# Optimization experiments

Measured on AMD Instinct MI355X. Metric: run time of the kernel, lower is better.

The kernel has to match this reference:

```python
import jax, jax.numpy as jnp
import numpy as np

EPS = 1e-5

def layernorm(x, g, b):
    mu = jnp.mean(x, axis=-1, keepdims=True)
    var = jnp.var(x, axis=-1, keepdims=True)
    return (x - mu) * jax.lax.rsqrt(var + EPS) * g + b

DIM = 1024; CTX = 1024; HEADS = 12; DHEAD = 64; INNER = HEADS * DHEAD
B = 4; F = 2048; J = 1024

def setup_inputs() -> dict:
    key = jax.random.key(0)
    ks = jax.random.split(key, 8)
    s = lambda d: 1.0 / np.sqrt(d)
    return {
        "x": jax.random.normal(ks[0], (B, F, DIM), jnp.float32),
        "tab_x": jax.random.normal(ks[1], (B, J, CTX), jnp.float32),
        "tab_g": jnp.ones((CTX,), jnp.float32), "tab_b": jnp.zeros((CTX,), jnp.float32),
        "vid_g": jnp.ones((DIM,), jnp.float32), "vid_b": jnp.zeros((DIM,), jnp.float32),
        "Wq": jax.random.normal(ks[2], (DIM, INNER), jnp.float32) * s(DIM),
        "Wk": jax.random.normal(ks[3], (CTX, INNER), jnp.float32) * s(CTX),
        "Wv": jax.random.normal(ks[4], (CTX, INNER), jnp.float32) * s(CTX),
        "q_g": jnp.ones((INNER,), jnp.float32), "q_b": jnp.zeros((INNER,), jnp.float32),
        "k_g": jnp.ones((INNER,), jnp.float32), "k_b": jnp.zeros((INNER,), jnp.float32),
        "Wo": jax.random.normal(ks[5], (INNER, DIM), jnp.float32) * s(INNER),
        "bo": jnp.zeros((DIM,), jnp.float32),
    }

def reference(x, tab_x, tab_g, tab_b, vid_g, vid_b, Wq, Wk, Wv, q_g, q_b, k_g, k_b, Wo, bo):
    scale = DHEAD ** -0.5
    kv_in = layernorm(tab_x, tab_g, tab_b)                      # [b,j,ctx]
    q = layernorm(layernorm(x, vid_g, vid_b) @ Wq, q_g, q_b)    # [b,f,inner]
    k = layernorm(kv_in @ Wk, k_g, k_b)                         # [b,j,inner]
    v = kv_in @ Wv                                              # [b,j,inner]
    split = lambda t: t.reshape(t.shape[0], t.shape[1], HEADS, DHEAD).transpose(0, 2, 1, 3)
    q, k, v = split(q) * scale, split(k), split(v)              # [b,h,*,d]
    sim = jnp.einsum('bhid,bhjd->bhij', q, k)
    attn = jax.nn.softmax(sim, axis=-1)
    out = jnp.einsum('bhij,bhjd->bhid', attn, v)                # [b,h,f,d]
    out = out.transpose(0, 2, 1, 3).reshape(x.shape[0], x.shape[1], INNER)
    return out @ Wo + bo
```

## Files before the change

### kernel.cpp

```cpp
#include <hip/hip_runtime.h>

typedef unsigned short u16;
typedef float  f32x4   __attribute__((ext_vector_type(4)));
typedef float  f32x16  __attribute__((ext_vector_type(16)));
typedef __bf16 bf16x8  __attribute__((ext_vector_type(8)));
typedef u16    u16x4   __attribute__((ext_vector_type(4)));

#define DEV __device__ __forceinline__

DEV u16 f2bf(float f) {
  union { float f; unsigned u; } x; x.f = f;
  unsigned r = x.u + 0x7fffu + ((x.u >> 16) & 1u);
  return (u16)(r >> 16);
}
DEV float bf2f(u16 b) { union { unsigned u; float f; } c; c.u = (unsigned)b << 16; return c.f; }

DEV unsigned cvtpk(float lo, float hi) {
  unsigned r;
  asm("v_cvt_pk_bf16_f32 %0, %1, %2" : "=v"(r) : "v"(lo), "v"(hi));
  return r;
}

DEV f32x4 mfma16(bf16x8 a, bf16x8 b, f32x4 c) {
  return __builtin_amdgcn_mfma_f32_16x16x32_bf16(a, b, c, 0, 0, 0);
}
DEV f32x16 mfma32(bf16x8 a, bf16x8 b, f32x16 c) {
  return __builtin_amdgcn_mfma_f32_32x32x16_bf16(a, b, c, 0, 0, 0);
}

DEV void gload16(const void* g, void* l) {
  __builtin_amdgcn_global_load_lds(
      (__attribute__((address_space(1))) void*)g,
      (__attribute__((address_space(3))) void*)l, 16, 0, 0);
}

template<typename LOADER>
DEV void ln_body(LOADER load, const float* __restrict__ g, const float* __restrict__ bta,
                 u16* __restrict__ yrow, int C, float outscale, float* red)
{
  const int tid = threadIdx.x;
  const int n4 = C >> 2;
  f32x4 v = {0.f, 0.f, 0.f, 0.f};
  if (tid < n4) v = load(tid);
  float s1 = v[0] + v[1] + v[2] + v[3];
  float s2 = v[0]*v[0] + v[1]*v[1] + v[2]*v[2] + v[3]*v[3];
#pragma unroll
  for (int o = 32; o > 0; o >>= 1) {
    s1 += __shfl_xor(s1, o, 64);
    s2 += __shfl_xor(s2, o, 64);
  }
  const int lane = tid & 63, wv = tid >> 6;
  if (lane == 0) { red[wv] = s1; red[4 + wv] = s2; }
  __syncthreads();
  s1 = red[0] + red[1] + red[2] + red[3];
  s2 = red[4] + red[5] + red[6] + red[7];
  const float mu = s1 / C;
  const float rs = rsqrtf(s2 / C - mu * mu + 1e-5f);
  if (tid < n4) {
    f32x4 gg = *(const f32x4*)(g + 4 * tid);
    f32x4 bb = *(const f32x4*)(bta + 4 * tid);
    u16x4 o4;
#pragma unroll
    for (int j = 0; j < 4; ++j)
      o4[j] = f2bf(((v[j] - mu) * rs * gg[j] + bb[j]) * outscale);
    *(u16x4*)(yrow + 4 * tid) = o4;
  }
}

__global__ __launch_bounds__(256)
void prep(const float* __restrict__ Wq, const float* __restrict__ Wk,
          const float* __restrict__ Wv, const float* __restrict__ Wo,
          u16* __restrict__ WqT, u16* __restrict__ WkvT, u16* __restrict__ WoT,
          const float* __restrict__ tabx, const float* __restrict__ tab_g,
          const float* __restrict__ tab_b,
          const float* __restrict__ x, const float* __restrict__ vid_g,
          const float* __restrict__ vid_b,
          u16* __restrict__ kvn, u16* __restrict__ xn)
{
  __shared__ float t[32][33];
  __shared__ float red[8];
  const int bid = blockIdx.x;
  const int tid = threadIdx.x;
  if (bid < 3840) {
    const float* src; u16* dst; int K, N, k0, n0;
    if (bid < 3072) {
      const int w = bid / 768, r = bid % 768;
      src = (w == 0) ? Wq : (w == 1) ? Wk : Wv;
      dst = (w == 0) ? WqT : (w == 1) ? WkvT : WkvT + (size_t)768 * 1024;
      K = 1024; N = 768; k0 = (r % 32) * 32; n0 = (r / 32) * 32;
    } else {
      const int r = bid - 3072;
      src = Wo; dst = WoT;
      K = 768; N = 1024; k0 = (r % 24) * 32; n0 = (r / 24) * 32;
    }
    const int tx = tid & 31, ty = tid >> 5;
#pragma unroll
    for (int i = ty; i < 32; i += 8)
      t[i][tx] = src[(size_t)(k0 + i) * N + n0 + tx];
    __syncthreads();
#pragma unroll
    for (int i = ty; i < 32; i += 8)
      dst[(size_t)(n0 + i) * K + k0 + tx] = f2bf(t[tx][i]);
  } else {
    const int r = bid - 3840;
    const float* xr; const float *g, *bb; u16* y;
    if (r < 4096) { xr = tabx + (size_t)r * 1024; g = tab_g; bb = tab_b;
                    y = kvn + (size_t)r * 1024; }
    else { const int rr = r - 4096; xr = x + (size_t)rr * 1024; g = vid_g;
           bb = vid_b; y = xn + (size_t)rr * 1024; }
    ln_body([&](int i) { return *(const f32x4*)(xr + 4 * i); }, g, bb, y, 1024, 1.0f, red);
  }
}

__global__ __launch_bounds__(256)
void gemm_qkv(const u16* __restrict__ xn, const u16* __restrict__ kvn,
              const u16* __restrict__ WqT, const u16* __restrict__ WkvT,
              u16* __restrict__ q_pre, u16* __restrict__ k_pre, u16* __restrict__ vb)
{
  __shared__ __align__(16) u16 As[2][64 * 64];
  __shared__ __align__(16) u16 Bs[2][128 * 64];
  const int bid = blockIdx.x;
  const int tid  = threadIdx.x;
  const int lane = tid & 63;
  const int wave = tid >> 6;
  const bool isq = bid >= 768;
  const u16* A; const u16* Bt; int bm, bn;
  if (!isq) { A = kvn;  Bt = WkvT; bm = (bid & 63) * 64;  bn = (bid >> 6) * 128; }
  else { const int r = bid - 768; A = xn; Bt = WqT; bm = (r & 127) * 64; bn = (r >> 7) * 128; }
  const int wm = (wave >> 1) * 32;
  const int wn = (wave & 1) * 64;
  const int fr = lane & 15;
  const int fk = (lane >> 4) * 8;

  f32x4 acc[2][4] = {};
  const char* gA0 = (const char*)(A  + (size_t)bm * 1024);
  const char* gB0 = (const char*)(Bt + (size_t)bn * 1024);
  const size_t rowpitch = 2048;

  auto stage = [&](int buf, int k0) {
#pragma unroll
    for (int c = 0; c < 2; ++c) {
      const int off = tid * 16 + c * 4096;
      gload16(gA0 + (size_t)(off >> 7) * rowpitch + 2 * k0 + (off & 127),
              (char*)&As[buf][0] + wave * 1024 + c * 4096);
    }
#pragma unroll
    for (int c = 0; c < 4; ++c) {
      const int off = tid * 16 + c * 4096;
      gload16(gB0 + (size_t)(off >> 7) * rowpitch + 2 * k0 + (off & 127),
              (char*)&Bs[buf][0] + wave * 1024 + c * 4096);
    }
  };

  stage(0, 0);
  __syncthreads();
  int cur = 0;
  for (int t = 0; t < 16; ++t) {
    if (t + 1 < 16) stage(cur ^ 1, (t + 1) * 64);
    bf16x8 af[2][2], bg[4][2];
#pragma unroll
    for (int m = 0; m < 2; ++m)
#pragma unroll
      for (int kk = 0; kk < 2; ++kk)
        af[m][kk] = *(const bf16x8*)&As[cur][(wm + m * 16 + fr) * 64 + kk * 32 + fk];
#pragma unroll
    for (int n = 0; n < 4; ++n)
#pragma unroll
      for (int kk = 0; kk < 2; ++kk)
        bg[n][kk] = *(const bf16x8*)&Bs[cur][(wn + n * 16 + fr) * 64 + kk * 32 + fk];
#pragma unroll
    for (int kk = 0; kk < 2; ++kk)
#pragma unroll
      for (int m = 0; m < 2; ++m)
#pragma unroll
        for (int n = 0; n < 4; ++n)
          acc[m][n] = mfma16(af[m][kk], bg[n][kk], acc[m][n]);
    if (t + 1 < 16) __syncthreads();
    cur ^= 1;
  }

  const int orow0 = bm + wm + 4 * (lane >> 4);
  const int ocol0 = bn + wn + fr;
#pragma unroll
  for (int m = 0; m < 2; ++m)
#pragma unroll
    for (int n = 0; n < 4; ++n)
#pragma unroll
      for (int r = 0; r < 4; ++r) {
        const int row = orow0 + m * 16 + r;
        const int col = ocol0 + n * 16;
        const u16 v = f2bf(acc[m][n][r]);
        if (isq) q_pre[(size_t)row * 768 + col] = v;
        else if (bn < 768) k_pre[(size_t)row * 768 + col] = v;
        else               vb[(size_t)row * 768 + (col - 768)] = v;
      }
}

__global__ __launch_bounds__(256)
void ln_tv(const u16* __restrict__ k_pre, const float* __restrict__ k_g,
           const float* __restrict__ k_b, u16* __restrict__ kb,
           const u16* __restrict__ q_pre, const float* __restrict__ q_g,
           const float* __restrict__ q_b, u16* __restrict__ qb,
           const u16* __restrict__ vb, u16* __restrict__ vT)
{
  __shared__ u16 t[64][65];
  __shared__ float red[8];
  const int bid = blockIdx.x;
  const int tid = threadIdx.x;
  if (bid < 12288) {
    const bool isk = bid < 4096;
    const int row = isk ? bid : bid - 4096;
    const u16* xr = (isk ? k_pre : q_pre) + (size_t)row * 768;
    u16* y = (isk ? kb : qb) + (size_t)row * 768;
    const float sc = isk ? 1.0f : 0.125f * 1.44269504089f;
    ln_body([&](int i) {
      const u16x4 raw = *(const u16x4*)(xr + 4 * i);
      f32x4 v; 
#pragma unroll
      for (int j = 0; j < 4; ++j) v[j] = bf2f(raw[j]);
      return v;
    }, isk ? k_g : q_g, isk ? k_b : q_b, y, 768, sc, red);
  } else {
    const int r2 = bid - 12288;
    const int bh = r2 % 48, b = bh / 12, h = bh - b * 12;
    const int j0 = (r2 / 48) * 64;
    const int tx = tid & 63, ty = tid >> 6;
#pragma unroll
    for (int i = ty; i < 64; i += 4)
      t[i][tx] = vb[(size_t)(b * 1024 + j0 + i) * 768 + h * 64 + tx];
    __syncthreads();
#pragma unroll
    for (int i = ty; i < 64; i += 4)
      vT[((size_t)bh * 64 + i) * 1024 + j0 + tx] = t[tx][i];
  }
}

__global__ __launch_bounds__(256, 3)
void attn4(const u16* __restrict__ q, const u16* __restrict__ k,
           const u16* __restrict__ vT, u16* __restrict__ att)
{
  __shared__ __align__(16) u16 Ks[2][64 * 64];
  __shared__ __align__(16) u16 Vs[2][64 * 64];
  __shared__ __align__(16) u16 osm[4][32][72];

  const int bh = blockIdx.x;
  const int b = bh / 12, h = bh - b * 12;
  const int tid = threadIdx.x, lane = tid & 63, wave = tid >> 6;
  const int lq  = lane & 31;
  const int hi5 = lane >> 5;
  const int qrow = blockIdx.y * 128 + wave * 32 + lq;

  const u16* qp = q + (size_t)(b * 2048 + qrow) * 768 + h * 64 + hi5 * 8;
  bf16x8 qf[4];
#pragma unroll
  for (int ds = 0; ds < 4; ++ds) qf[ds] = *(const bf16x8*)(qp + ds * 16);

  f32x16 ot0 = {}, ot1 = {};
  float m = -1e30f, l = 0.f;

  const char* kg = (const char*)k + (size_t)(b * 1024) * 1536 + h * 128;
  const char* vg = (const char*)vT + (size_t)bh * 64 * 2048;
  const int rsw0 = (lq & 7) << 4;

  auto stage = [&](int buf, int j0) {
#pragma unroll
    for (int c = 0; c < 2; ++c) {
      const int o   = tid * 16 + c * 4096;
      const int row = o >> 7;
      const int scol = (o & 127) ^ ((row & 7) << 4);
      gload16(kg + (size_t)(j0 + row) * 1536 + scol,
              (char*)&Ks[buf][0] + wave * 1024 + c * 4096);
      gload16(vg + (size_t)row * 2048 + j0 * 2 + scol,
              (char*)&Vs[buf][0] + wave * 1024 + c * 4096);
    }
  };

  stage(0, 0);
  __syncthreads();
  int cur = 0;
  for (int t = 0; t < 16; ++t) {
    const int j0 = t * 64;
    if (t + 1 < 16) stage(cur ^ 1, j0 + 64);
    f32x16 st0 = {}, st1 = {};
    __builtin_amdgcn_s_setprio(1);
#pragma unroll
    for (int ds = 0; ds < 4; ++ds) {
      const int cb = ds * 32 + hi5 * 16;
      const bf16x8 k0 = *(const bf16x8*)((const char*)&Ks[cur][0] + lq * 128 + (cb ^ rsw0));
      const bf16x8 k1 = *(const bf16x8*)((const char*)&Ks[cur][0] + (lq + 32) * 128 + (cb ^ rsw0));
      st0 = mfma32(k0, qf[ds], st0);
      st1 = mfma32(k1, qf[ds], st1);
    }
    __builtin_amdgcn_s_setprio(0);
    float ta0 = fmaxf(st0[0], st1[0]), ta1 = fmaxf(st0[1], st1[1]);
    float ta2 = fmaxf(st0[2], st1[2]), ta3 = fmaxf(st0[3], st1[3]);
#pragma unroll
    for (int r = 4; r < 16; r += 4) {
      ta0 = fmaxf(fmaxf(st0[r],     st1[r]),     ta0);
      ta1 = fmaxf(fmaxf(st0[r + 1], st1[r + 1]), ta1);
      ta2 = fmaxf(fmaxf(st0[r + 2], st1[r + 2]), ta2);
      ta3 = fmaxf(fmaxf(st0[r + 3], st1[r + 3]), ta3);
    }
    float tmax = fmaxf(fmaxf(fmaxf(ta0, ta1), ta2), ta3);
    tmax = fmaxf(tmax, __shfl_xor(tmax, 32, 64));
    if (!__all(tmax - m <= 11.5416f)) {
      const float mn = fmaxf(m, tmax);
      const float sc = exp2f(m - mn);
      l *= sc;
#pragma unroll
      for (int r = 0; r < 16; ++r) { ot0[r] *= sc; ot1[r] *= sc; }
      m = mn;
    }
    float sa0 = 0.f, sa1 = 0.f, sa2 = 0.f, sa3 = 0.f;
#pragma unroll
    for (int r = 0; r < 16; r += 4) {
      float p0 = exp2f(st0[r]     - m); st0[r]     = p0; sa0 += p0;
      float p1 = exp2f(st0[r + 1] - m); st0[r + 1] = p1; sa1 += p1;
      float p2 = exp2f(st0[r + 2] - m); st0[r + 2] = p2; sa2 += p2;
      float p3 = exp2f(st0[r + 3] - m); st0[r + 3] = p3; sa3 += p3;
    }
#pragma unroll
    for (int r = 0; r < 16; r += 4) {
      float p0 = exp2f(st1[r]     - m); st1[r]     = p0; sa0 += p0;
      float p1 = exp2f(st1[r + 1] - m); st1[r + 1] = p1; sa1 += p1;
      float p2 = exp2f(st1[r + 2] - m); st1[r + 2] = p2; sa2 += p2;
      float p3 = exp2f(st1[r + 3] - m); st1[r + 3] = p3; sa3 += p3;
    }
    float ts = (sa0 + sa1) + (sa2 + sa3);
    ts += __shfl_xor(ts, 32, 64);
    l += ts;
    __builtin_amdgcn_s_setprio(1);
#pragma unroll
    for (int s4 = 0; s4 < 4; ++s4) {
      const int u = (s4 & 1) * 8;
      float a0, a1, a2, a3, b0, b1, b2, b3;
      if (s4 < 2) {
        a0 = st0[u]; a1 = st0[u + 1]; a2 = st0[u + 2]; a3 = st0[u + 3];
        b0 = st0[u + 4]; b1 = st0[u + 5]; b2 = st0[u + 6]; b3 = st0[u + 7];
      } else {
        a0 = st1[u]; a1 = st1[u + 1]; a2 = st1[u + 2]; a3 = st1[u + 3];
        b0 = st1[u + 4]; b1 = st1[u + 5]; b2 = st1[u + 6]; b3 = st1[u + 7];
      }
      const unsigned L0 = cvtpk(a0, a1), L1 = cvtpk(a2, a3);
      const unsigned H0 = cvtpk(b0, b1), H1 = cvtpk(b2, b3);
      const auto w02 = __builtin_amdgcn_permlane32_swap(L0, H0, false, false);
      const auto w13 = __builtin_amdgcn_permlane32_swap(L1, H1, false, false);
      union BU { unsigned w[4]; bf16x8 v; } pu;
      pu.w[0] = w02[0]; pu.w[1] = w13[0]; pu.w[2] = w02[1]; pu.w[3] = w13[1];
      const int cb = s4 * 32 + hi5 * 16;
      const bf16x8 v0 = *(const bf16x8*)((const char*)&Vs[cur][0] + lq * 128 + (cb ^ rsw0));
      const bf16x8 v1 = *(const bf16x8*)((const char*)&Vs[cur][0] + (lq + 32) * 128 + (cb ^ rsw0));
      ot0 = mfma32(v0, pu.v, ot0);
      ot1 = mfma32(v1, pu.v, ot1);
    }
    __builtin_amdgcn_s_setprio(0);
    if (t + 1 < 16) __syncthreads();
    cur ^= 1;
  }
  const float inv = 1.0f / l;
#pragma unroll
  for (int r = 0; r < 16; ++r) {
    const int d0 = (r & 3) + 8 * (r >> 2) + 4 * hi5;
    osm[wave][lq][d0]      = f2bf(ot0[r] * inv);
    osm[wave][lq][32 + d0] = f2bf(ot1[r] * inv);
  }
  __syncthreads();
  const int col = (lane & 7) * 8;
#pragma unroll
  for (int pass = 0; pass < 4; ++pass) {
    const int row = pass * 8 + (lane >> 3);
    const bf16x8 vv = *(const bf16x8*)&osm[wave][row][col];
    const int qg = blockIdx.y * 128 + wave * 32 + row;
    *(bf16x8*)(att + (size_t)(b * 2048 + qg) * 768 + h * 64 + col) = vv;
  }
}

__global__ __launch_bounds__(256)
void gemm_o(const u16* __restrict__ A, const u16* __restrict__ Bt,
            float* __restrict__ Cp, const float* __restrict__ bias)
{
  __shared__ __align__(16) u16 As[2][64 * 64];
  __shared__ __align__(16) u16 Bs[2][128 * 64];
  const int tid  = threadIdx.x;
  const int lane = tid & 63;
  const int wave = tid >> 6;
  const int bm = blockIdx.x * 64;
  const int bn = blockIdx.y * 128;
  const int wm = (wave >> 1) * 32;
  const int wn = (wave & 1) * 64;
  const int fr = lane & 15;
  const int fk = (lane >> 4) * 8;

  f32x4 acc[2][4] = {};
  const char* gA0 = (const char*)(A  + (size_t)bm * 768);
  const char* gB0 = (const char*)(Bt + (size_t)bn * 768);
  const size_t rowpitch = 1536;

  auto stage = [&](int buf, int k0) {
#pragma unroll
    for (int c = 0; c < 2; ++c) {
      const int off = tid * 16 + c * 4096;
      gload16(gA0 + (size_t)(off >> 7) * rowpitch + 2 * k0 + (off & 127),
              (char*)&As[buf][0] + wave * 1024 + c * 4096);
    }
#pragma unroll
    for (int c = 0; c < 4; ++c) {
      const int off = tid * 16 + c * 4096;
      gload16(gB0 + (size_t)(off >> 7) * rowpitch + 2 * k0 + (off & 127),
              (char*)&Bs[buf][0] + wave * 1024 + c * 4096);
    }
  };

  stage(0, 0);
  __syncthreads();
  int cur = 0;
  for (int t = 0; t < 12; ++t) {
    if (t + 1 < 12) stage(cur ^ 1, (t + 1) * 64);
    bf16x8 af[2][2], bg[4][2];
#pragma unroll
    for (int m = 0; m < 2; ++m)
#pragma unroll
      for (int kk = 0; kk < 2; ++kk)
        af[m][kk] = *(const bf16x8*)&As[cur][(wm + m * 16 + fr) * 64 + kk * 32 + fk];
#pragma unroll
    for (int n = 0; n < 4; ++n)
#pragma unroll
      for (int kk = 0; kk < 2; ++kk)
        bg[n][kk] = *(const bf16x8*)&Bs[cur][(wn + n * 16 + fr) * 64 + kk * 32 + fk];
#pragma unroll
    for (int kk = 0; kk < 2; ++kk)
#pragma unroll
      for (int m = 0; m < 2; ++m)
#pragma unroll
        for (int n = 0; n < 4; ++n)
          acc[m][n] = mfma16(af[m][kk], bg[n][kk], acc[m][n]);
    if (t + 1 < 12) __syncthreads();
    cur ^= 1;
  }

  const int orow0 = bm + wm + 4 * (lane >> 4);
  const int ocol0 = bn + wn + fr;
#pragma unroll
  for (int m = 0; m < 2; ++m)
#pragma unroll
    for (int n = 0; n < 4; ++n)
#pragma unroll
      for (int r = 0; r < 4; ++r) {
        const int row = orow0 + m * 16 + r;
        const int col = ocol0 + n * 16;
        Cp[(size_t)row * 1024 + col] = acc[m][n][r] + bias[col];
      }
}

extern "C" void kernel_launch(void* const* d_in, const int* in_sizes, int n_in,
                              void* d_out, int out_size, void* d_ws, size_t ws_size,
                              hipStream_t stream)
{
  const float* x     = (const float*)d_in[0];
  const float* tabx  = (const float*)d_in[1];
  const float* tab_g = (const float*)d_in[2];
  const float* tab_b = (const float*)d_in[3];
  const float* vid_g = (const float*)d_in[4];
  const float* vid_b = (const float*)d_in[5];
  const float* Wq    = (const float*)d_in[6];
  const float* Wk    = (const float*)d_in[7];
  const float* Wv    = (const float*)d_in[8];
  const float* q_g   = (const float*)d_in[9];
  const float* q_b   = (const float*)d_in[10];
  const float* k_g   = (const float*)d_in[11];
  const float* k_b   = (const float*)d_in[12];
  const float* Wo    = (const float*)d_in[13];
  const float* bo    = (const float*)d_in[14];

  char* ws = (char*)d_ws;
  const size_t O_WQT  = 0;
  const size_t O_WKVT = O_WQT  + (size_t)768 * 1024 * 2;
  const size_t O_WOT  = O_WKVT + (size_t)1536 * 1024 * 2;
  const size_t O_XN   = O_WOT  + (size_t)1024 * 768 * 2;
  const size_t O_KVN  = O_XN   + (size_t)8192 * 1024 * 2;
  const size_t O_QPRE = O_KVN  + (size_t)4096 * 1024 * 2;
  const size_t O_KPRE = O_QPRE + (size_t)8192 * 768 * 2;
  const size_t O_QB   = O_KPRE + (size_t)4096 * 768 * 2;
  const size_t O_KB   = O_QB   + (size_t)8192 * 768 * 2;
  const size_t O_VB   = O_KB   + (size_t)4096 * 768 * 2;
  const size_t O_VT   = O_VB   + (size_t)4096 * 768 * 2;
  const size_t O_ATT  = O_QPRE;

  u16*   WqT   = (u16*)(ws + O_WQT);
  u16*   WkvT  = (u16*)(ws + O_WKVT);
  u16*   WoT   = (u16*)(ws + O_WOT);
  u16*   xn    = (u16*)(ws + O_XN);
  u16*   kvn   = (u16*)(ws + O_KVN);
  u16*   q_pre = (u16*)(ws + O_QPRE);
  u16*   k_pre = (u16*)(ws + O_KPRE);
  u16*   qb    = (u16*)(ws + O_QB);
  u16*   kb    = (u16*)(ws + O_KB);
  u16*   vb    = (u16*)(ws + O_VB);
  u16*   vT    = (u16*)(ws + O_VT);
  u16*   attb  = (u16*)(ws + O_ATT);

  prep<<<16128, 256, 0, stream>>>(Wq, Wk, Wv, Wo, WqT, WkvT, WoT,
                                  tabx, tab_g, tab_b, x, vid_g, vid_b, kvn, xn);
  gemm_qkv<<<1536, 256, 0, stream>>>(xn, kvn, WqT, WkvT, q_pre, k_pre, vb);
  ln_tv<<<13056, 256, 0, stream>>>(k_pre, k_g, k_b, kb, q_pre, q_g, q_b, qb, vb, vT);
  attn4<<<dim3(48, 16), 256, 0, stream>>>(qb, kb, vT, attb);
  gemm_o<<<dim3(128, 8), 256, 0, stream>>>(attb, WoT, (float*)d_out, bo);
}
```

Baseline: 156.9 us.

## Swizzle GEMM LDS tiles, write V transposed from GEMM, relax pipeline barriers

The QKV and output GEMMs now XOR-swizzle their LDS tiles to avoid bank conflicts on fragment reads. The QKV GEMM writes V directly in the transposed per-head layout, which removes the separate transpose pass and the vb buffer. All three main loops switch from __syncthreads to explicit vmcnt waits plus raw s_barrier so prefetches stay in flight. The attention epilogue replaces a block barrier with an lgkmcnt wait. This risks subtle sync bugs if the vmcnt counts are wrong, and the transposed V stores are strided 8-byte writes.

```diff
diff --git a/kernel.cpp b/kernel.cpp
--- a/kernel.cpp
+++ b/kernel.cpp
@@ -115,7 +115,7 @@
 __global__ __launch_bounds__(256)
 void gemm_qkv(const u16* __restrict__ xn, const u16* __restrict__ kvn,
               const u16* __restrict__ WqT, const u16* __restrict__ WkvT,
-              u16* __restrict__ q_pre, u16* __restrict__ k_pre, u16* __restrict__ vb)
+              u16* __restrict__ q_pre, u16* __restrict__ k_pre, u16* __restrict__ vT)
 {
   __shared__ __align__(16) u16 As[2][64 * 64];
   __shared__ __align__(16) u16 Bs[2][128 * 64];
@@ -130,7 +130,7 @@
   const int wm = (wave >> 1) * 32;
   const int wn = (wave & 1) * 64;
   const int fr = lane & 15;
-  const int fk = (lane >> 4) * 8;
+  const int fkb = (lane >> 4) * 16;
 
   f32x4 acc[2][4] = {};
   const char* gA0 = (const char*)(A  + (size_t)bm * 1024);
@@ -141,33 +141,39 @@
 #pragma unroll
     for (int c = 0; c < 2; ++c) {
       const int off = tid * 16 + c * 4096;
-      gload16(gA0 + (size_t)(off >> 7) * rowpitch + 2 * k0 + (off & 127),
+      const int row = off >> 7;
+      const int scol = (off & 127) ^ ((row & 7) << 4);
+      gload16(gA0 + (size_t)row * rowpitch + 2 * k0 + scol,
               (char*)&As[buf][0] + wave * 1024 + c * 4096);
     }
 #pragma unroll
     for (int c = 0; c < 4; ++c) {
       const int off = tid * 16 + c * 4096;
-      gload16(gB0 + (size_t)(off >> 7) * rowpitch + 2 * k0 + (off & 127),
+      const int row = off >> 7;
+      const int scol = (off & 127) ^ ((row & 7) << 4);
+      gload16(gB0 + (size_t)row * rowpitch + 2 * k0 + scol,
               (char*)&Bs[buf][0] + wave * 1024 + c * 4096);
     }
   };
 
-  stage(0, 0);
-  __syncthreads();
-  int cur = 0;
-  for (int t = 0; t < 16; ++t) {
-    if (t + 1 < 16) stage(cur ^ 1, (t + 1) * 64);
+  auto step = [&](int cur) {
     bf16x8 af[2][2], bg[4][2];
 #pragma unroll
     for (int m = 0; m < 2; ++m)
 #pragma unroll
-      for (int kk = 0; kk < 2; ++kk)
-        af[m][kk] = *(const bf16x8*)&As[cur][(wm + m * 16 + fr) * 64 + kk * 32 + fk];
+      for (int kk = 0; kk < 2; ++kk) {
+        const int row = wm + m * 16 + fr;
+        af[m][kk] = *(const bf16x8*)((const char*)&As[cur][0] + row * 128 +
+                                     ((kk * 64 + fkb) ^ ((row & 7) << 4)));
+      }
 #pragma unroll
     for (int n = 0; n < 4; ++n)
 #pragma unroll
-      for (int kk = 0; kk < 2; ++kk)
-        bg[n][kk] = *(const bf16x8*)&Bs[cur][(wn + n * 16 + fr) * 64 + kk * 32 + fk];
+      for (int kk = 0; kk < 2; ++kk) {
+        const int row = wn + n * 16 + fr;
+        bg[n][kk] = *(const bf16x8*)((const char*)&Bs[cur][0] + row * 128 +
+                                     ((kk * 64 + fkb) ^ ((row & 7) << 4)));
+      }
 #pragma unroll
     for (int kk = 0; kk < 2; ++kk)
 #pragma unroll
@@ -175,68 +181,73 @@
 #pragma unroll
         for (int n = 0; n < 4; ++n)
           acc[m][n] = mfma16(af[m][kk], bg[n][kk], acc[m][n]);
-    if (t + 1 < 16) __syncthreads();
-    cur ^= 1;
-  }
+  };
+
+  stage(0, 0);
+#pragma unroll 1
+  for (int t = 0; t < 15; ++t) {
+    stage((t & 1) ^ 1, (t + 1) * 64);
+    asm volatile("s_waitcnt vmcnt(6)" ::: "memory");
+    __builtin_amdgcn_s_barrier();
+    step(t & 1);
+    __builtin_amdgcn_s_barrier();
+    asm volatile("" ::: "memory");
+  }
+  asm volatile("s_waitcnt vmcnt(0)" ::: "memory");
+  __builtin_amdgcn_s_barrier();
+  step(15 & 1);
 
   const int orow0 = bm + wm + 4 * (lane >> 4);
   const int ocol0 = bn + wn + fr;
 #pragma unroll
   for (int m = 0; m < 2; ++m)
 #pragma unroll
-    for (int n = 0; n < 4; ++n)
-#pragma unroll
-      for (int r = 0; r < 4; ++r) {
-        const int row = orow0 + m * 16 + r;
-        const int col = ocol0 + n * 16;
-        const u16 v = f2bf(acc[m][n][r]);
-        if (isq) q_pre[(size_t)row * 768 + col] = v;
-        else if (bn < 768) k_pre[(size_t)row * 768 + col] = v;
-        else               vb[(size_t)row * 768 + (col - 768)] = v;
-      }
+    for (int n = 0; n < 4; ++n) {
+      const int row0 = orow0 + m * 16;
+      const int col  = ocol0 + n * 16;
+      if (isq) {
+#pragma unroll
+        for (int r = 0; r < 4; ++r)
+          q_pre[(size_t)(row0 + r) * 768 + col] = f2bf(acc[m][n][r]);
+      } else if (bn < 768) {
+#pragma unroll
+        for (int r = 0; r < 4; ++r)
+          k_pre[(size_t)(row0 + r) * 768 + col] = f2bf(acc[m][n][r]);
+      } else {
+        const int c2 = col - 768, hh = c2 >> 6, dd = c2 & 63;
+        const int bb2 = row0 >> 10, jj = row0 & 1023;
+        u16x4 o4;
+#pragma unroll
+        for (int r = 0; r < 4; ++r) o4[r] = f2bf(acc[m][n][r]);
+        *(u16x4*)(vT + ((size_t)(bb2 * 12 + hh) * 64 + dd) * 1024 + jj) = o4;
+      }
+    }
 }
 
 __global__ __launch_bounds__(256)
-void ln_tv(const u16* __restrict__ k_pre, const float* __restrict__ k_g,
+void ln_qk(const u16* __restrict__ k_pre, const float* __restrict__ k_g,
            const float* __restrict__ k_b, u16* __restrict__ kb,
            const u16* __restrict__ q_pre, const float* __restrict__ q_g,
-           const float* __restrict__ q_b, u16* __restrict__ qb,
-           const u16* __restrict__ vb, u16* __restrict__ vT)
-{
-  __shared__ u16 t[64][65];
+           const float* __restrict__ q_b, u16* __restrict__ qb)
+{
   __shared__ float red[8];
   const int bid = blockIdx.x;
-  const int tid = threadIdx.x;
-  if (bid < 12288) {
-    const bool isk = bid < 4096;
-    const int row = isk ? bid : bid - 4096;
-    const u16* xr = (isk ? k_pre : q_pre) + (size_t)row * 768;
-    u16* y = (isk ? kb : qb) + (size_t)row * 768;
-    const float sc = isk ? 1.0f : 0.125f * 1.44269504089f;
-    ln_body([&](int i) {
-      const u16x4 raw = *(const u16x4*)(xr + 4 * i);
-      f32x4 v; 
-#pragma unroll
-      for (int j = 0; j < 4; ++j) v[j] = bf2f(raw[j]);
-      return v;
-    }, isk ? k_g : q_g, isk ? k_b : q_b, y, 768, sc, red);
-  } else {
-    const int r2 = bid - 12288;
-    const int bh = r2 % 48, b = bh / 12, h = bh - b * 12;
-    const int j0 = (r2 / 48) * 64;
-    const int tx = tid & 63, ty = tid >> 6;
-#pragma unroll
-    for (int i = ty; i < 64; i += 4)
-      t[i][tx] = vb[(size_t)(b * 1024 + j0 + i) * 768 + h * 64 + tx];
-    __syncthreads();
-#pragma unroll
-    for (int i = ty; i < 64; i += 4)
-      vT[((size_t)bh * 64 + i) * 1024 + j0 + tx] = t[tx][i];
-  }
+  const bool isk = bid < 4096;
+  const int row = isk ? bid : bid - 4096;
+  const u16* xr = (isk ? k_pre : q_pre) + (size_t)row * 768;
+  u16* y = (isk ? kb : qb) + (size_t)row * 768;
+  const float sc = isk ? 1.0f : 0.125f * 1.44269504089f;
+  ln_body([&](int i) {
+    const u16x4 raw = *(const u16x4*)(xr + 4 * i);
+    f32x4 v;
+#pragma unroll
+    for (int j = 0; j < 4; ++j) v[j] = bf2f(raw[j]);
+    return v;
+  }, isk ? k_g : q_g, isk ? k_b : q_b, y, 768, sc, red);
 }
 
 __global__ __launch_bounds__(256, 3)
-void attn4(const u16* __restrict__ q, const u16* __restrict__ k,
+void attn6(const u16* __restrict__ q, const u16* __restrict__ k,
            const u16* __restrict__ vT, u16* __restrict__ att)
 {
   __shared__ __align__(16) u16 Ks[2][64 * 64];
@@ -270,17 +281,12 @@
       const int scol = (o & 127) ^ ((row & 7) << 4);
       gload16(kg + (size_t)(j0 + row) * 1536 + scol,
               (char*)&Ks[buf][0] + wave * 1024 + c * 4096);
-      gload16(vg + (size_t)row * 2048 + j0 * 2 + scol,
+      gload16(vg + (size_t)row * 2048 + (size_t)j0 * 2 + scol,
               (char*)&Vs[buf][0] + wave * 1024 + c * 4096);
     }
   };
 
-  stage(0, 0);
-  __syncthreads();
-  int cur = 0;
-  for (int t = 0; t < 16; ++t) {
-    const int j0 = t * 64;
-    if (t + 1 < 16) stage(cur ^ 1, j0 + 64);
+  auto step = [&](int cur) {
     f32x16 st0 = {}, st1 = {};
     __builtin_amdgcn_s_setprio(1);
 #pragma unroll
@@ -354,9 +360,22 @@
       ot1 = mfma32(v1, pu.v, ot1);
     }
     __builtin_amdgcn_s_setprio(0);
-    if (t + 1 < 16) __syncthreads();
-    cur ^= 1;
-  }
+  };
+
+  stage(0, 0);
+#pragma unroll 1
+  for (int t = 0; t < 15; ++t) {
+    stage((t & 1) ^ 1, (t + 1) * 64);
+    asm volatile("s_waitcnt vmcnt(4)" ::: "memory");
+    __builtin_amdgcn_s_barrier();
+    step(t & 1);
+    __builtin_amdgcn_s_barrier();
+    asm volatile("" ::: "memory");
+  }
+  asm volatile("s_waitcnt vmcnt(0)" ::: "memory");
+  __builtin_amdgcn_s_barrier();
+  step(15 & 1);
+
   const float inv = 1.0f / l;
 #pragma unroll
   for (int r = 0; r < 16; ++r) {
@@ -364,7 +383,7 @@
     osm[wave][lq][d0]      = f2bf(ot0[r] * inv);
     osm[wave][lq][32 + d0] = f2bf(ot1[r] * inv);
   }
-  __syncthreads();
+  asm volatile("s_waitcnt lgkmcnt(0)" ::: "memory");
   const int col = (lane & 7) * 8;
 #pragma unroll
   for (int pass = 0; pass < 4; ++pass) {
@@ -389,7 +408,7 @@
   const int wm = (wave >> 1) * 32;
   const int wn = (wave & 1) * 64;
   const int fr = lane & 15;
-  const int fk = (lane >> 4) * 8;
+  const int fkb = (lane >> 4) * 16;
 
   f32x4 acc[2][4] = {};
   const char* gA0 = (const char*)(A  + (size_t)bm * 768);
@@ -400,33 +419,39 @@
 #pragma unroll
     for (int c = 0; c < 2; ++c) {
       const int off = tid * 16 + c * 4096;
-      gload16(gA0 + (size_t)(off >> 7) * rowpitch + 2 * k0 + (off & 127),
+      const int row = off >> 7;
+      const int scol = (off & 127) ^ ((row & 7) << 4);
+      gload16(gA0 + (size_t)row * rowpitch + 2 * k0 + scol,
               (char*)&As[buf][0] + wave * 1024 + c * 4096);
     }
 #pragma unroll
     for (int c = 0; c < 4; ++c) {
       const int off = tid * 16 + c * 4096;
-      gload16(gB0 + (size_t)(off >> 7) * rowpitch + 2 * k0 + (off & 127),
+      const int row = off >> 7;
+      const int scol = (off & 127) ^ ((row & 7) << 4);
+      gload16(gB0 + (size_t)row * rowpitch + 2 * k0 + scol,
               (char*)&Bs[buf][0] + wave * 1024 + c * 4096);
     }
   };
 
-  stage(0, 0);
-  __syncthreads();
-  int cur = 0;
-  for (int t = 0; t < 12; ++t) {
-    if (t + 1 < 12) stage(cur ^ 1, (t + 1) * 64);
+  auto step = [&](int cur) {
     bf16x8 af[2][2], bg[4][2];
 #pragma unroll
     for (int m = 0; m < 2; ++m)
 #pragma unroll
-      for (int kk = 0; kk < 2; ++kk)
-        af[m][kk] = *(const bf16x8*)&As[cur][(wm + m * 16 + fr) * 64 + kk * 32 + fk];
+      for (int kk = 0; kk < 2; ++kk) {
+        const int row = wm + m * 16 + fr;
+        af[m][kk] = *(const bf16x8*)((const char*)&As[cur][0] + row * 128 +
+                                     ((kk * 64 + fkb) ^ ((row & 7) << 4)));
+      }
 #pragma unroll
     for (int n = 0; n < 4; ++n)
 #pragma unroll
-      for (int kk = 0; kk < 2; ++kk)
-        bg[n][kk] = *(const bf16x8*)&Bs[cur][(wn + n * 16 + fr) * 64 + kk * 32 + fk];
+      for (int kk = 0; kk < 2; ++kk) {
+        const int row = wn + n * 16 + fr;
+        bg[n][kk] = *(const bf16x8*)((const char*)&Bs[cur][0] + row * 128 +
+                                     ((kk * 64 + fkb) ^ ((row & 7) << 4)));
+      }
 #pragma unroll
     for (int kk = 0; kk < 2; ++kk)
 #pragma unroll
@@ -434,9 +459,21 @@
 #pragma unroll
         for (int n = 0; n < 4; ++n)
           acc[m][n] = mfma16(af[m][kk], bg[n][kk], acc[m][n]);
-    if (t + 1 < 12) __syncthreads();
-    cur ^= 1;
-  }
+  };
+
+  stage(0, 0);
+#pragma unroll 1
+  for (int t = 0; t < 11; ++t) {
+    stage((t & 1) ^ 1, (t + 1) * 64);
+    asm volatile("s_waitcnt vmcnt(6)" ::: "memory");
+    __builtin_amdgcn_s_barrier();
+    step(t & 1);
+    __builtin_amdgcn_s_barrier();
+    asm volatile("" ::: "memory");
+  }
+  asm volatile("s_waitcnt vmcnt(0)" ::: "memory");
+  __builtin_amdgcn_s_barrier();
+  step(11 & 1);
 
   const int orow0 = bm + wm + 4 * (lane >> 4);
   const int ocol0 = bn + wn + fr;
@@ -482,8 +519,7 @@
   const size_t O_KPRE = O_QPRE + (size_t)8192 * 768 * 2;
   const size_t O_QB   = O_KPRE + (size_t)4096 * 768 * 2;
   const size_t O_KB   = O_QB   + (size_t)8192 * 768 * 2;
-  const size_t O_VB   = O_KB   + (size_t)4096 * 768 * 2;
-  const size_t O_VT   = O_VB   + (size_t)4096 * 768 * 2;
+  const size_t O_VT   = O_KB   + (size_t)4096 * 768 * 2;
   const size_t O_ATT  = O_QPRE;
 
   u16*   WqT   = (u16*)(ws + O_WQT);
@@ -495,14 +531,13 @@
   u16*   k_pre = (u16*)(ws + O_KPRE);
   u16*   qb    = (u16*)(ws + O_QB);
   u16*   kb    = (u16*)(ws + O_KB);
-  u16*   vb    = (u16*)(ws + O_VB);
   u16*   vT    = (u16*)(ws + O_VT);
   u16*   attb  = (u16*)(ws + O_ATT);
 
   prep<<<16128, 256, 0, stream>>>(Wq, Wk, Wv, Wo, WqT, WkvT, WoT,
                                   tabx, tab_g, tab_b, x, vid_g, vid_b, kvn, xn);
-  gemm_qkv<<<1536, 256, 0, stream>>>(xn, kvn, WqT, WkvT, q_pre, k_pre, vb);
-  ln_tv<<<13056, 256, 0, stream>>>(k_pre, k_g, k_b, kb, q_pre, q_g, q_b, qb, vb, vT);
-  attn4<<<dim3(48, 16), 256, 0, stream>>>(qb, kb, vT, attb);
+  gemm_qkv<<<1536, 256, 0, stream>>>(xn, kvn, WqT, WkvT, q_pre, k_pre, vT);
+  ln_qk<<<12288, 256, 0, stream>>>(k_pre, k_g, k_b, kb, q_pre, q_g, q_b, qb);
+  attn6<<<dim3(48, 16), 256, 0, stream>>>(qb, kb, vT, attb);
   gemm_o<<<dim3(128, 8), 256, 0, stream>>>(attb, WoT, (float*)d_out, bo);
 }
```

Measured after the change: 140.0 us. -10.8%, faster.
